# Kernel optimization log

Hardware: AMD Instinct MI355X
Metric: run time of the kernel (lower is better)

Reference implementation:

```python
import jax, jax.numpy as jnp
import numpy as np

B, T, C = 4, 2048, 1024
NH = 16
HD = C // NH  # 64

def setup_inputs() -> dict:
    key = jax.random.key(0)
    k1, k2, k3 = jax.random.split(key, 3)
    x = jax.random.normal(k1, (B, T, C), dtype=jnp.float32)
    w_qkv = jax.random.normal(k2, (C, 3 * C), dtype=jnp.float32) * (1.0 / np.sqrt(C))
    w_out = jax.random.normal(k3, (C, C), dtype=jnp.float32) * (1.0 / np.sqrt(C))
    b_out = jnp.zeros((C,), dtype=jnp.float32)
    return {"x": x, "w_qkv": w_qkv, "w_out": w_out, "b_out": b_out}

def reference(x, w_qkv, w_out, b_out):
    b, t, c = x.shape
    nh, hd = NH, c // NH
    qkv = x @ w_qkv                      # [b, t, 3c]
    q, k, v = jnp.split(qkv, 3, axis=-1)
    # [b, t, c] -> [b, nh, t, hd]
    def heads(z):
        return z.reshape(b, t, nh, hd).transpose(0, 2, 1, 3)
    q, k, v = heads(q), heads(k), heads(v)
    scale = 1.0 / jnp.sqrt(jnp.asarray(hd, dtype=x.dtype))
    scores = jnp.einsum('bhqd,bhkd->bhqk', q, k) * scale  # [b, nh, t, t]
    causal = jnp.tril(jnp.ones((t, t), dtype=bool))
    scores = jnp.where(causal, scores, jnp.asarray(-jnp.inf, dtype=scores.dtype))
    attn = jax.nn.softmax(scores, axis=-1)
    ctx = jnp.einsum('bhqk,bhkd->bhqd', attn, v)           # [b, nh, t, hd]
    ctx = ctx.transpose(0, 2, 1, 3).reshape(b, t, c)
    return ctx @ w_out + b_out
```

## Files before the change

kernel.cpp:

```cpp
#include <hip/hip_runtime.h>
#include <cmath>


typedef __bf16 bf16x4 __attribute__((ext_vector_type(4)));
typedef __bf16 bf16x8 __attribute__((ext_vector_type(8)));
typedef float  f32x4  __attribute__((ext_vector_type(4)));

__device__ __forceinline__ void gload_lds16(const __bf16* g, __bf16* l) {
    __builtin_amdgcn_global_load_lds(
        (const __attribute__((address_space(1))) void*)g,
        (__attribute__((address_space(3))) void*)l,
        16, 0, 0);
}

__global__ __launch_bounds__(256) void cast_bf16(const float* __restrict__ in,
                                                 __bf16* __restrict__ out, int n4) {
    int i = blockIdx.x * 256 + threadIdx.x;
    if (i >= n4) return;
    float4 f = *(const float4*)(in + (size_t)i * 4);
    bf16x4 o;
    o[0] = (__bf16)f.x; o[1] = (__bf16)f.y; o[2] = (__bf16)f.z; o[3] = (__bf16)f.w;
    *(bf16x4*)(out + (size_t)i * 4) = o;
}

__global__ __launch_bounds__(256) void transpose_cast(const float* __restrict__ W,
                                                      __bf16* __restrict__ WT,
                                                      int K, int N) {
    __shared__ float tile[32][33];
    const int n0 = blockIdx.x * 32, k0 = blockIdx.y * 32;
    const int tx = threadIdx.x & 31, ty = threadIdx.x >> 5;
    #pragma unroll
    for (int i = 0; i < 4; ++i)
        tile[ty + 8 * i][tx] = W[(size_t)(k0 + ty + 8 * i) * N + n0 + tx];
    __syncthreads();
    #pragma unroll
    for (int i = 0; i < 4; ++i)
        WT[(size_t)(n0 + ty + 8 * i) * K + k0 + tx] = (__bf16)tile[tx][ty + 8 * i];
}

__global__ __launch_bounds__(256) void transpose_v(const __bf16* __restrict__ qkv,
                                                   __bf16* __restrict__ Vt) {
    constexpr int T = 2048, R3C = 3072;
    __shared__ __bf16 tile[64][72];
    const int bh = blockIdx.y;
    const int b  = bh >> 4, h = bh & 15;
    const int kt = blockIdx.x * 64;
    const int tid = threadIdx.x;
    #pragma unroll
    for (int i = 0; i < 2; ++i) {
        int idx = tid + 256 * i;
        int kr  = idx >> 3;
        int c8  = idx & 7;
        *(uint4*)&tile[kr][c8 * 8] =
            *(const uint4*)(qkv + (size_t)(b * T + kt + kr) * R3C + 2048 + h * 64 + c8 * 8);
    }
    __syncthreads();
    #pragma unroll
    for (int i = 0; i < 2; ++i) {
        int idx = tid + 256 * i;
        int d   = idx >> 3;
        int k8  = idx & 7;
        union { __bf16 v[8]; uint4 u; } t;
        #pragma unroll
        for (int j = 0; j < 8; ++j) t.v[j] = tile[k8 * 8 + j][d];
        *(uint4*)(Vt + ((size_t)bh * 64 + d) * T + kt + k8 * 8) = t.u;
    }
}

template <typename OutT, bool BIAS>
__global__ __launch_bounds__(256) void gemm_bt(const __bf16* __restrict__ A,
                                               const __bf16* __restrict__ BT,
                                               OutT* __restrict__ Cc,
                                               const float* __restrict__ bias,
                                               int M, int N, int K) {
    __shared__ __bf16 As[128 * 32];
    __shared__ __bf16 Bs[128 * 32];

    const int tid  = threadIdx.x;
    const int lane = tid & 63;
    const int w    = tid >> 6;
    const int wr   = w >> 1, wc = w & 1;
    const int cc   = lane & 15, gg = lane >> 4;
    const int rowBase = blockIdx.y * 128;
    const int colBase = blockIdx.x * 128;

    f32x4 acc[4][4];
    #pragma unroll
    for (int i = 0; i < 4; ++i)
        #pragma unroll
        for (int j = 0; j < 4; ++j) acc[i][j] = f32x4{0.f, 0.f, 0.f, 0.f};

    for (int k0 = 0; k0 < K; k0 += 32) {
        __syncthreads();
        #pragma unroll
        for (int i = 0; i < 2; ++i) {
            int idx = tid + 256 * i;
            int r   = idx >> 2;
            int c4  = idx & 3;
            gload_lds16(A  + (size_t)(rowBase + r) * K + k0 + c4 * 8, &As[idx * 8]);
            gload_lds16(BT + (size_t)(colBase + r) * K + k0 + c4 * 8, &Bs[idx * 8]);
        }
        __syncthreads();

        bf16x8 af[4], bfr[4];
        #pragma unroll
        for (int i = 0; i < 4; ++i)
            af[i] = *(const bf16x8*)&As[(wr * 64 + i * 16 + cc) * 32 + gg * 8];
        #pragma unroll
        for (int j = 0; j < 4; ++j)
            bfr[j] = *(const bf16x8*)&Bs[(wc * 64 + j * 16 + cc) * 32 + gg * 8];
        #pragma unroll
        for (int i = 0; i < 4; ++i)
            #pragma unroll
            for (int j = 0; j < 4; ++j)
                acc[i][j] = __builtin_amdgcn_mfma_f32_16x16x32_bf16(af[i], bfr[j], acc[i][j], 0, 0, 0);
    }

    #pragma unroll
    for (int i = 0; i < 4; ++i)
        #pragma unroll
        for (int j = 0; j < 4; ++j) {
            const int col = colBase + wc * 64 + j * 16 + cc;
            #pragma unroll
            for (int r = 0; r < 4; ++r) {
                const int row = rowBase + wr * 64 + i * 16 + gg * 4 + r;
                float v = acc[i][j][r];
                if (BIAS) v += bias[col];
                Cc[(size_t)row * N + col] = (OutT)v;
            }
        }
}

__global__ __launch_bounds__(256) void flash_attn_mfma(const __bf16* __restrict__ qkv,
                                                       const __bf16* __restrict__ Vt,
                                                       __bf16* __restrict__ ctx) {
    constexpr int T = 2048, C = 1024, NH = 16, HD = 64;
    constexpr int R3C = 3 * C;
    constexpr float K1 = 0.125f * 1.44269504088896f;
    constexpr float K2 = -16.0f * 1.44269504088896f;

    const int tid  = threadIdx.x;
    const int lane = tid & 63;
    const int w    = tid >> 6;
    const int c    = lane & 15;
    const int g    = lane >> 4;

    const int bh    = blockIdx.x;
    const int qt    = 15 - (int)blockIdx.y;
    const int b     = bh >> 4;
    const int h     = bh & 15;
    const int qbase = qt * 128;

    __shared__ __attribute__((aligned(16))) __bf16 Ks [64][72];
    __shared__ __attribute__((aligned(16))) __bf16 VsT[64][72];
    __shared__ __attribute__((aligned(16))) __bf16 Ps [4][32][72];

    const __bf16* Qhead = qkv + (size_t)(b * T) * R3C + h * HD;
    bf16x8 Qa[2][2];
    #pragma unroll
    for (int st = 0; st < 2; ++st)
        #pragma unroll
        for (int ks = 0; ks < 2; ++ks)
            Qa[st][ks] = *(const bf16x8*)(Qhead +
                (size_t)(qbase + w * 32 + st * 16 + c) * R3C + ks * 32 + g * 8);

    f32x4 O0[4], O1[4], L0, L1;
    #pragma unroll
    for (int n = 0; n < 4; ++n) { O0[n] = f32x4{0.f,0.f,0.f,0.f}; O1[n] = f32x4{0.f,0.f,0.f,0.f}; }
    L0 = f32x4{0.f,0.f,0.f,0.f}; L1 = f32x4{0.f,0.f,0.f,0.f};

    bf16x8 ones;
    #pragma unroll
    for (int j = 0; j < 8; ++j) ones[j] = (__bf16)1.0f;

    const __bf16* Kb  = qkv + (size_t)(b * T) * R3C + C + h * HD;
    const __bf16* Vtb = Vt + (size_t)bh * 64 * T;

    const int srow0 = qbase + w * 32;
    const int srow1 = srow0 + 16;
    const int ktmax = qbase + 64;

    for (int kt = 0; kt <= ktmax; kt += 64) {
        __syncthreads();
        #pragma unroll
        for (int i = 0; i < 2; ++i) {
            int idx = tid + 256 * i;
            int kr  = idx >> 3;
            int c8  = idx & 7;
            *(uint4*)&Ks[kr][c8 * 8] = *(const uint4*)(Kb + (size_t)(kt + kr) * R3C + c8 * 8);
        }
        #pragma unroll
        for (int i = 0; i < 2; ++i) {
            int idx = tid + 256 * i;
            int d   = idx >> 3;
            int k8  = idx & 7;
            *(uint4*)&VsT[d][k8 * 8] = *(const uint4*)(Vtb + (size_t)d * T + kt + k8 * 8);
        }
        __syncthreads();

        f32x4 S0[4], S1[4];
        #pragma unroll
        for (int s = 0; s < 4; ++s) { S0[s] = f32x4{0.f,0.f,0.f,0.f}; S1[s] = f32x4{0.f,0.f,0.f,0.f}; }
        #pragma unroll
        for (int ks = 0; ks < 2; ++ks)
            #pragma unroll
            for (int sub = 0; sub < 4; ++sub) {
                bf16x8 kb = *(const bf16x8*)&Ks[sub * 16 + c][ks * 32 + g * 8];
                S0[sub] = __builtin_amdgcn_mfma_f32_16x16x32_bf16(Qa[0][ks], kb, S0[sub], 0, 0, 0);
                S1[sub] = __builtin_amdgcn_mfma_f32_16x16x32_bf16(Qa[1][ks], kb, S1[sub], 0, 0, 0);
            }
        if (kt + 63 > srow0) {
            #pragma unroll
            for (int sub = 0; sub < 4; ++sub) {
                int key = kt + sub * 16 + c;
                #pragma unroll
                for (int r = 0; r < 4; ++r)
                    if (key > srow0 + g * 4 + r) S0[sub][r] = -1e30f;
            }
        }
        if (kt + 63 > srow1) {
            #pragma unroll
            for (int sub = 0; sub < 4; ++sub) {
                int key = kt + sub * 16 + c;
                #pragma unroll
                for (int r = 0; r < 4; ++r)
                    if (key > srow1 + g * 4 + r) S1[sub][r] = -1e30f;
            }
        }
        #pragma unroll
        for (int sub = 0; sub < 4; ++sub)
            #pragma unroll
            for (int r = 0; r < 4; ++r) {
                float p0 = exp2f(fmaf(S0[sub][r], K1, K2));
                float p1 = exp2f(fmaf(S1[sub][r], K1, K2));
                Ps[w][g * 4 + r]     [sub * 16 + c] = (__bf16)p0;
                Ps[w][16 + g * 4 + r][sub * 16 + c] = (__bf16)p1;
            }

        #pragma unroll
        for (int ks = 0; ks < 2; ++ks) {
            bf16x8 pa0 = *(const bf16x8*)&Ps[w][c]     [ks * 32 + g * 8];
            bf16x8 pa1 = *(const bf16x8*)&Ps[w][16 + c][ks * 32 + g * 8];
            #pragma unroll
            for (int n = 0; n < 4; ++n) {
                bf16x8 vb = *(const bf16x8*)&VsT[n * 16 + c][ks * 32 + g * 8];
                O0[n] = __builtin_amdgcn_mfma_f32_16x16x32_bf16(pa0, vb, O0[n], 0, 0, 0);
                O1[n] = __builtin_amdgcn_mfma_f32_16x16x32_bf16(pa1, vb, O1[n], 0, 0, 0);
            }
            L0 = __builtin_amdgcn_mfma_f32_16x16x32_bf16(pa0, ones, L0, 0, 0, 0);
            L1 = __builtin_amdgcn_mfma_f32_16x16x32_bf16(pa1, ones, L1, 0, 0, 0);
        }
    }

    float i0[4], i1[4];
    #pragma unroll
    for (int r = 0; r < 4; ++r) { i0[r] = 1.f / L0[r]; i1[r] = 1.f / L1[r]; }
    #pragma unroll
    for (int n = 0; n < 4; ++n)
        #pragma unroll
        for (int r = 0; r < 4; ++r) {
            size_t row0 = (size_t)(b * T + srow0 + g * 4 + r);
            size_t row1 = (size_t)(b * T + srow1 + g * 4 + r);
            ctx[row0 * C + h * HD + n * 16 + c] = (__bf16)(O0[n][r] * i0[r]);
            ctx[row1 * C + h * HD + n * 16 + c] = (__bf16)(O1[n][r] * i1[r]);
        }
}

extern "C" void kernel_launch(void* const* d_in, const int* in_sizes, int n_in,
                              void* d_out, int out_size, void* d_ws, size_t ws_size,
                              hipStream_t stream) {
    constexpr int B = 4, T = 2048, C = 1024;
    constexpr int M = B * T;

    const float* x     = (const float*)d_in[0];
    const float* w_qkv = (const float*)d_in[1];
    const float* w_out = (const float*)d_in[2];
    const float* b_out = (const float*)d_in[3];
    float* out = (float*)d_out;

    char* ws = (char*)d_ws;
    __bf16* xb     = (__bf16*)(ws);
    __bf16* wqkvT  = (__bf16*)(ws + (16ull << 20));
    __bf16* woutT  = (__bf16*)(ws + (22ull << 20));
    __bf16* qkvb   = (__bf16*)(ws + (24ull << 20));
    __bf16* ctxb   = (__bf16*)(ws + (72ull << 20));
    __bf16* Vt     = (__bf16*)(ws + (88ull << 20));

    cast_bf16<<<(M * C / 4 + 255) / 256, 256, 0, stream>>>(x, xb, M * C / 4);
    transpose_cast<<<dim3(3 * C / 32, C / 32), 256, 0, stream>>>(w_qkv, wqkvT, C, 3 * C);
    transpose_cast<<<dim3(C / 32, C / 32), 256, 0, stream>>>(w_out, woutT, C, C);

    gemm_bt<__bf16, false><<<dim3(3 * C / 128, M / 128), 256, 0, stream>>>(
        xb, wqkvT, qkvb, nullptr, M, 3 * C, C);

    transpose_v<<<dim3(T / 64, B * 16), 256, 0, stream>>>(qkvb, Vt);

    flash_attn_mfma<<<dim3(B * 16, T / 128), 256, 0, stream>>>(qkvb, Vt, ctxb);

    gemm_bt<float, true><<<dim3(C / 128, M / 128), 256, 0, stream>>>(
        ctxb, woutT, out, b_out, M, C, C);
}
```

Before: 310.5 us.

## Switch flash attention to 32x32x16 MFMA with transposed S and scalar row sums

Rewrites the attention inner loop to use 32x32x16 bf16 MFMA instructions, computing S transposed (K as the A operand, Q as B) so that each lane owns one query row. The row sum of P is now accumulated with scalar adds in registers plus one cross-half shuffle, replacing the extra MFMA against a ones vector. P is written to LDS as packed 4-element stores and the output as vectorised row stores. The aim is fewer MFMA and LDS instructions per tile. The cost is larger per-lane accumulators and a different causal-mask index mapping.

```diff
diff --git a/kernel.cpp b/kernel.cpp
--- a/kernel.cpp
+++ b/kernel.cpp
@@ -5,6 +5,7 @@
 typedef __bf16 bf16x4 __attribute__((ext_vector_type(4)));
 typedef __bf16 bf16x8 __attribute__((ext_vector_type(8)));
 typedef float  f32x4  __attribute__((ext_vector_type(4)));
+typedef float  f32x16 __attribute__((ext_vector_type(16)));
 
 __device__ __forceinline__ void gload_lds16(const __bf16* g, __bf16* l) {
     __builtin_amdgcn_global_load_lds(
@@ -142,42 +143,36 @@
     const int tid  = threadIdx.x;
     const int lane = tid & 63;
     const int w    = tid >> 6;
-    const int c    = lane & 15;
-    const int g    = lane >> 4;
+    const int q5   = lane & 31;
+    const int half = lane >> 5;
 
     const int bh    = blockIdx.x;
     const int qt    = 15 - (int)blockIdx.y;
     const int b     = bh >> 4;
     const int h     = bh & 15;
     const int qbase = qt * 128;
+    const int srow  = qbase + w * 32;
 
     __shared__ __attribute__((aligned(16))) __bf16 Ks [64][72];
     __shared__ __attribute__((aligned(16))) __bf16 VsT[64][72];
     __shared__ __attribute__((aligned(16))) __bf16 Ps [4][32][72];
 
-    const __bf16* Qhead = qkv + (size_t)(b * T) * R3C + h * HD;
-    bf16x8 Qa[2][2];
-    #pragma unroll
-    for (int st = 0; st < 2; ++st)
-        #pragma unroll
-        for (int ks = 0; ks < 2; ++ks)
-            Qa[st][ks] = *(const bf16x8*)(Qhead +
-                (size_t)(qbase + w * 32 + st * 16 + c) * R3C + ks * 32 + g * 8);
-
-    f32x4 O0[4], O1[4], L0, L1;
-    #pragma unroll
-    for (int n = 0; n < 4; ++n) { O0[n] = f32x4{0.f,0.f,0.f,0.f}; O1[n] = f32x4{0.f,0.f,0.f,0.f}; }
-    L0 = f32x4{0.f,0.f,0.f,0.f}; L1 = f32x4{0.f,0.f,0.f,0.f};
-
-    bf16x8 ones;
-    #pragma unroll
-    for (int j = 0; j < 8; ++j) ones[j] = (__bf16)1.0f;
+    const __bf16* Qrow = qkv + (size_t)(b * T + srow + q5) * R3C + h * HD;
+    bf16x8 Qb[4];
+    #pragma unroll
+    for (int ks = 0; ks < 4; ++ks)
+        Qb[ks] = *(const bf16x8*)(Qrow + ks * 16 + half * 8);
+
+    f32x16 O[2];
+    #pragma unroll
+    for (int mb = 0; mb < 2; ++mb)
+        #pragma unroll
+        for (int r = 0; r < 16; ++r) O[mb][r] = 0.f;
+    float lsum = 0.f;
 
     const __bf16* Kb  = qkv + (size_t)(b * T) * R3C + C + h * HD;
     const __bf16* Vtb = Vt + (size_t)bh * 64 * T;
 
-    const int srow0 = qbase + w * 32;
-    const int srow1 = srow0 + 16;
     const int ktmax = qbase + 64;
 
     for (int kt = 0; kt <= ktmax; kt += 64) {
@@ -198,71 +193,59 @@
         }
         __syncthreads();
 
-        f32x4 S0[4], S1[4];
-        #pragma unroll
-        for (int s = 0; s < 4; ++s) { S0[s] = f32x4{0.f,0.f,0.f,0.f}; S1[s] = f32x4{0.f,0.f,0.f,0.f}; }
-        #pragma unroll
-        for (int ks = 0; ks < 2; ++ks)
-            #pragma unroll
-            for (int sub = 0; sub < 4; ++sub) {
-                bf16x8 kb = *(const bf16x8*)&Ks[sub * 16 + c][ks * 32 + g * 8];
-                S0[sub] = __builtin_amdgcn_mfma_f32_16x16x32_bf16(Qa[0][ks], kb, S0[sub], 0, 0, 0);
-                S1[sub] = __builtin_amdgcn_mfma_f32_16x16x32_bf16(Qa[1][ks], kb, S1[sub], 0, 0, 0);
-            }
-        if (kt + 63 > srow0) {
-            #pragma unroll
-            for (int sub = 0; sub < 4; ++sub) {
-                int key = kt + sub * 16 + c;
+        #pragma unroll
+        for (int sub = 0; sub < 2; ++sub) {
+            f32x16 S;
+            #pragma unroll
+            for (int r = 0; r < 16; ++r) S[r] = 0.f;
+            #pragma unroll
+            for (int ks = 0; ks < 4; ++ks) {
+                bf16x8 kb = *(const bf16x8*)&Ks[sub * 32 + q5][ks * 16 + half * 8];
+                S = __builtin_amdgcn_mfma_f32_32x32x16_bf16(kb, Qb[ks], S, 0, 0, 0);
+            }
+            if (kt + sub * 32 + 31 > srow) {
                 #pragma unroll
-                for (int r = 0; r < 4; ++r)
-                    if (key > srow0 + g * 4 + r) S0[sub][r] = -1e30f;
-            }
-        }
-        if (kt + 63 > srow1) {
-            #pragma unroll
-            for (int sub = 0; sub < 4; ++sub) {
-                int key = kt + sub * 16 + c;
+                for (int r = 0; r < 16; ++r) {
+                    int key = kt + sub * 32 + (r & 3) + 8 * (r >> 2) + 4 * half;
+                    if (key > srow + q5) S[r] = -1e30f;
+                }
+            }
+            #pragma unroll
+            for (int a = 0; a < 4; ++a) {
+                union { bf16x4 v; uint2 u; } pk;
                 #pragma unroll
-                for (int r = 0; r < 4; ++r)
-                    if (key > srow1 + g * 4 + r) S1[sub][r] = -1e30f;
-            }
-        }
-        #pragma unroll
-        for (int sub = 0; sub < 4; ++sub)
-            #pragma unroll
-            for (int r = 0; r < 4; ++r) {
-                float p0 = exp2f(fmaf(S0[sub][r], K1, K2));
-                float p1 = exp2f(fmaf(S1[sub][r], K1, K2));
-                Ps[w][g * 4 + r]     [sub * 16 + c] = (__bf16)p0;
-                Ps[w][16 + g * 4 + r][sub * 16 + c] = (__bf16)p1;
-            }
-
-        #pragma unroll
-        for (int ks = 0; ks < 2; ++ks) {
-            bf16x8 pa0 = *(const bf16x8*)&Ps[w][c]     [ks * 32 + g * 8];
-            bf16x8 pa1 = *(const bf16x8*)&Ps[w][16 + c][ks * 32 + g * 8];
-            #pragma unroll
-            for (int n = 0; n < 4; ++n) {
-                bf16x8 vb = *(const bf16x8*)&VsT[n * 16 + c][ks * 32 + g * 8];
-                O0[n] = __builtin_amdgcn_mfma_f32_16x16x32_bf16(pa0, vb, O0[n], 0, 0, 0);
-                O1[n] = __builtin_amdgcn_mfma_f32_16x16x32_bf16(pa1, vb, O1[n], 0, 0, 0);
-            }
-            L0 = __builtin_amdgcn_mfma_f32_16x16x32_bf16(pa0, ones, L0, 0, 0, 0);
-            L1 = __builtin_amdgcn_mfma_f32_16x16x32_bf16(pa1, ones, L1, 0, 0, 0);
-        }
-    }
-
-    float i0[4], i1[4];
-    #pragma unroll
-    for (int r = 0; r < 4; ++r) { i0[r] = 1.f / L0[r]; i1[r] = 1.f / L1[r]; }
-    #pragma unroll
-    for (int n = 0; n < 4; ++n)
-        #pragma unroll
-        for (int r = 0; r < 4; ++r) {
-            size_t row0 = (size_t)(b * T + srow0 + g * 4 + r);
-            size_t row1 = (size_t)(b * T + srow1 + g * 4 + r);
-            ctx[row0 * C + h * HD + n * 16 + c] = (__bf16)(O0[n][r] * i0[r]);
-            ctx[row1 * C + h * HD + n * 16 + c] = (__bf16)(O1[n][r] * i1[r]);
+                for (int bq = 0; bq < 4; ++bq) {
+                    float p = exp2f(fmaf(S[4 * a + bq], K1, K2));
+                    lsum += p;
+                    pk.v[bq] = (__bf16)p;
+                }
+                *(uint2*)&Ps[w][q5][sub * 32 + 8 * a + 4 * half] = pk.u;
+            }
+        }
+
+        #pragma unroll
+        for (int ks2 = 0; ks2 < 4; ++ks2) {
+            bf16x8 pa = *(const bf16x8*)&Ps[w][q5][ks2 * 16 + half * 8];
+            #pragma unroll
+            for (int mb = 0; mb < 2; ++mb) {
+                bf16x8 vb = *(const bf16x8*)&VsT[mb * 32 + q5][ks2 * 16 + half * 8];
+                O[mb] = __builtin_amdgcn_mfma_f32_32x32x16_bf16(vb, pa, O[mb], 0, 0, 0);
+            }
+        }
+    }
+
+    const float inv = 1.f / (lsum + __shfl_xor(lsum, 32));
+
+    __bf16* crow = ctx + (size_t)(b * T + srow + q5) * C + h * HD;
+    #pragma unroll
+    for (int mb = 0; mb < 2; ++mb)
+        #pragma unroll
+        for (int a = 0; a < 4; ++a) {
+            union { bf16x4 v; uint2 u; } pk;
+            #pragma unroll
+            for (int bq = 0; bq < 4; ++bq)
+                pk.v[bq] = (__bf16)(O[mb][4 * a + bq] * inv);
+            *(uint2*)(crow + mb * 32 + 8 * a + 4 * half) = pk.u;
         }
 }
 
```

Result: faster. 289.8 us (-6.7%).
